# Kernel tuning notes

Hardware: AMD Instinct MI355X
Metric: run time of the kernel (lower is better)

Reference implementation:

```python
import jax, jax.numpy as jnp
import numpy as np


def setup_inputs() -> dict:
    key = jax.random.key(0)
    k1, k2, k3, k4 = jax.random.split(key, 4)
    n_smps, n_fcns, d_in, d_out = 16384, 2048, 32, 32
    GAIN = 1e-5  # xavier gain used by init_wts / init_offsets
    x = jax.random.normal(k1, (n_smps, d_in), dtype=jnp.float32)
    ctrs = jax.random.normal(k2, (n_fcns, d_in), dtype=jnp.float32)
    wts = jax.random.normal(k3, (n_fcns, d_in, d_out), dtype=jnp.float32) * GAIN
    offsets = jax.random.normal(k4, (n_fcns, d_out), dtype=jnp.float32) * GAIN
    return {"x": x, "ctrs": ctrs, "wts": wts, "offsets": offsets, "k": 4}


def reference(x, ctrs, wts, offsets, k):
    # --- knn_do equivalent (done under no_grad in torch) ---
    # squared Euclidean distance: (n_smps, n_fcns)
    x_sg = jax.lax.stop_gradient(x)
    c_sg = jax.lax.stop_gradient(ctrs)
    d2 = (jnp.sum(x_sg * x_sg, axis=1, keepdims=True)
          - 2.0 * (x_sg @ c_sg.T)
          + jnp.sum(c_sg * c_sg, axis=1)[None, :])
    _, idx = jax.lax.top_k(-d2, k)  # (n_smps, k), nearest centers

    # --- gather per-neighbor local linear models ---
    sel_wts = wts[idx]        # (n_smps, k, d_in, d_out)
    sel_ctrs = ctrs[idx]      # (n_smps, k, d_in)
    sel_offs = offsets[idx]   # (n_smps, k, d_out)

    applied_wts = jnp.sum(sel_wts, axis=1)  # (n_smps, d_in, d_out)
    # offsets minus sum over neighbors/d_in of wts * ctrs
    applied_offsets = (jnp.sum(sel_offs, axis=1)
                       - jnp.einsum('nkde,nkd->ne', sel_wts, sel_ctrs))
    # y = x @ applied_wts + applied_offsets, per sample
    y = jnp.einsum('nde,nd->ne', applied_wts, x) + applied_offsets
    return y
```

## Files before the change

kernel.cpp:

```cpp
#include <hip/hip_runtime.h>
#include <math.h>

typedef short bf16x8 __attribute__((ext_vector_type(8)));
typedef float f32x4  __attribute__((ext_vector_type(4)));

#define N_SMPS 16384
#define N_FCNS 2048
#define D_IN 32
#define D_OUT 32
#define KNN 4
#define SPLITS 4
#define CPS 512
#define TILES 32
#define POOL 48

__device__ __forceinline__ unsigned umin_u(unsigned a, unsigned b) { return a < b ? a : b; }
__device__ __forceinline__ unsigned umax_u(unsigned a, unsigned b) { return a > b ? a : b; }

__device__ __forceinline__ unsigned short bf16_rne(float f) {
  unsigned b = __float_as_uint(f);
  unsigned r = b + 0x7FFFu + ((b >> 16) & 1u);
  return (unsigned short)(r >> 16);
}

#define OFF_XH   0u
#define OFF_CH   1048576u
#define OFF_HB   (OFF_CH + 131072u)
#define OFF_WB   (OFF_HB + 8192u)
#define OFF_POOL (OFF_WB + 4194304u)

#define NX4 (N_SMPS * D_IN / 4)
#define NC4 (N_FCNS * D_IN / 4)
#define NW4 (N_FCNS * D_IN * D_OUT / 4)
#define NTOT (NX4 + NC4 + NW4)

__global__ __launch_bounds__(256) void k_prep(
    const float* __restrict__ x, const float* __restrict__ ctrs,
    const float* __restrict__ wts,
    unsigned short* __restrict__ xh, unsigned short* __restrict__ ch,
    unsigned short* __restrict__ wb, float* __restrict__ hb)
{
  const int gt = blockIdx.x * 256 + threadIdx.x;
  const float* src; unsigned short* dst; int i4;
  if (gt < NX4)            { src = x;    dst = xh; i4 = gt; }
  else if (gt < NX4 + NC4) { src = ctrs; dst = ch; i4 = gt - NX4; }
  else                     { src = wts;  dst = wb; i4 = gt - (NX4 + NC4); }
  float4 v = ((const float4*)src)[i4];
  ushort4 o;
  o.x = bf16_rne(v.x); o.y = bf16_rne(v.y);
  o.z = bf16_rne(v.z); o.w = bf16_rne(v.w);
  ((ushort4*)dst)[i4] = o;

  if (gt < N_FCNS) {
    const float4* cp4 = (const float4*)(ctrs + (size_t)gt * D_IN);
    float a = 0.f;
    #pragma unroll
    for (int q = 0; q < 8; ++q) {
      float4 c = cp4[q];
      a += c.x * c.x + c.y * c.y + c.z * c.z + c.w * c.w;
    }
    hb[gt] = -0.5f * a;
  }
}

__global__ __launch_bounds__(256) void k_topk(
    const unsigned short* __restrict__ xh, const unsigned short* __restrict__ ch,
    const float* __restrict__ hb, unsigned* __restrict__ pool)
{
  __shared__ unsigned s_cand[SPLITS][16][16][4];

  const int tid = threadIdx.x;
  const int lane = tid & 63;
  const int w = __builtin_amdgcn_readfirstlane(tid >> 6);
  const int col = lane & 15;
  const int quad = lane >> 4;
  const int sbase = blockIdx.x * 16;
  const int nbase0 = w * CPS;

  const bf16x8 ah =
      *(const bf16x8*)(xh + (size_t)(sbase + col) * D_IN + quad * 8);

  unsigned ls[4][4];
  #pragma unroll
  for (int r = 0; r < 4; ++r)
    #pragma unroll
    for (int e = 0; e < 4; ++e) ls[r][e] = 0u;

  const unsigned short* chb = ch + (size_t)nbase0 * D_IN + (size_t)col * D_IN + quad * 8;
  #define BLOAD(t) (*(const bf16x8*)(chb + (size_t)(t) * 16 * D_IN))
  #define HLOAD(t) (hb[nbase0 + (t) * 16 + col])

  bf16x8 bh0 = BLOAD(0), bh1 = BLOAD(1);
  float  hv0 = HLOAD(0), hv1 = HLOAD(1);

  for (int t = 0; t < TILES; t += 2) {
    const int tp0 = (t + 2) & (TILES - 1);
    const int tp1 = (t + 3) & (TILES - 1);
    bf16x8 bhn0 = BLOAD(tp0), bhn1 = BLOAD(tp1);
    float  hvn0 = HLOAD(tp0), hvn1 = HLOAD(tp1);

    {
      f32x4 acc = {0.f, 0.f, 0.f, 0.f};
      acc = __builtin_amdgcn_mfma_f32_16x16x32_bf16(ah, bh0, acc, 0, 0, 0);
      const unsigned tc = (unsigned)(t * 16 + col);
      #pragma unroll
      for (int r = 0; r < 4; ++r) {
        const float u = acc[r] + hv0;
        unsigned b = __float_as_uint(u);
        unsigned m = b ^ ((unsigned)((int)b >> 31) | 0x80000000u);
        unsigned key = (m & 0xFFFFFE00u) | tc;
        unsigned t0 = umin_u(ls[r][0], key); ls[r][0] = umax_u(ls[r][0], key);
        unsigned t1 = umin_u(ls[r][1], t0);  ls[r][1] = umax_u(ls[r][1], t0);
        unsigned t2 = umin_u(ls[r][2], t1);  ls[r][2] = umax_u(ls[r][2], t1);
        ls[r][3] = umax_u(ls[r][3], t2);
      }
    }
    {
      f32x4 acc = {0.f, 0.f, 0.f, 0.f};
      acc = __builtin_amdgcn_mfma_f32_16x16x32_bf16(ah, bh1, acc, 0, 0, 0);
      const unsigned tc = (unsigned)((t + 1) * 16 + col);
      #pragma unroll
      for (int r = 0; r < 4; ++r) {
        const float u = acc[r] + hv1;
        unsigned b = __float_as_uint(u);
        unsigned m = b ^ ((unsigned)((int)b >> 31) | 0x80000000u);
        unsigned key = (m & 0xFFFFFE00u) | tc;
        unsigned t0 = umin_u(ls[r][0], key); ls[r][0] = umax_u(ls[r][0], key);
        unsigned t1 = umin_u(ls[r][1], t0);  ls[r][1] = umax_u(ls[r][1], t0);
        unsigned t2 = umin_u(ls[r][2], t1);  ls[r][2] = umax_u(ls[r][2], t1);
        ls[r][3] = umax_u(ls[r][3], t2);
      }
    }
    bh0 = bhn0; bh1 = bhn1; hv0 = hvn0; hv1 = hvn1;
  }
  #undef BLOAD
  #undef HLOAD

  #pragma unroll
  for (int r = 0; r < 4; ++r) {
    const int row = quad * 4 + r;
    *(uint4*)&s_cand[w][row][col][0] =
        make_uint4(ls[r][0], ls[r][1], ls[r][2], ls[r][3]);
  }
  __syncthreads();

  if (tid < 128) {
    const int sl = tid >> 3;
    const int g  = tid & 7;
    const int wv = g >> 1;
    const int chh = (g & 1) * 8;
    unsigned q0 = 0, q1 = 0, q2 = 0, q3 = 0, q4 = 0, q5 = 0;
    #pragma unroll
    for (int c2 = 0; c2 < 8; ++c2) {
      uint4 kv = *(const uint4*)&s_cand[wv][sl][chh + c2][0];
      unsigned ks[4] = {kv.x, kv.y, kv.z, kv.w};
      #pragma unroll
      for (int e = 0; e < 4; ++e) {
        unsigned key = ks[e];
        unsigned t0 = umin_u(q0, key); q0 = umax_u(q0, key);
        unsigned t1 = umin_u(q1, t0);  q1 = umax_u(q1, t0);
        unsigned t2 = umin_u(q2, t1);  q2 = umax_u(q2, t1);
        unsigned t3 = umin_u(q3, t2);  q3 = umax_u(q3, t2);
        unsigned t4 = umin_u(q4, t3);  q4 = umax_u(q4, t3);
        q5 = umax_u(q5, t4);
      }
    }
    unsigned* op = pool + (size_t)(sbase + sl) * POOL + g * 6;
    op[0] = q0; op[1] = q1; op[2] = q2;
    op[3] = q3; op[4] = q4; op[5] = q5;
  }
}

#define K2_BLOCK 256
#define K2_SAMPLES 8

__global__ __launch_bounds__(K2_BLOCK) void k_apply(
    const float* __restrict__ x, const float* __restrict__ ctrs,
    const unsigned short* __restrict__ wb, const float* __restrict__ offs,
    const unsigned* __restrict__ pool, float* __restrict__ y)
{
  __shared__ double s_pd2[K2_SAMPLES][POOL];
  __shared__ int    s_pix[K2_SAMPLES][POOL];
  __shared__ int    s_sel[K2_SAMPLES][KNN];
  __shared__ float  s_diff[K2_SAMPLES][KNN][D_IN + 1];
  __shared__ float4 s_part[K2_SAMPLES][KNN][D_OUT / 4];

  const int tid = threadIdx.x;
  const int sbase = blockIdx.x * K2_SAMPLES;

  for (int c = tid; c < K2_SAMPLES * POOL; c += K2_BLOCK) {
    const int sl = c / POOL;
    const int p = c - sl * POOL;
    const unsigned key = pool[(size_t)(sbase + sl) * POOL + p];
    const int wv = p / 12;
    const int j = wv * CPS + (int)(key & 0x1FFu);
    const float4* xp4 = (const float4*)(x + (size_t)(sbase + sl) * D_IN);
    const float4* cp4 = (const float4*)(ctrs + (size_t)j * D_IN);
    double d2a = 0.0, d2b = 0.0;
    #pragma unroll
    for (int q = 0; q < 8; ++q) {
      float4 cv = cp4[q];
      float4 xv = xp4[q];
      double df0 = (double)xv.x - (double)cv.x;
      double df1 = (double)xv.y - (double)cv.y;
      double df2 = (double)xv.z - (double)cv.z;
      double df3 = (double)xv.w - (double)cv.w;
      d2a = fma(df0, df0, d2a);
      d2b = fma(df1, df1, d2b);
      d2a = fma(df2, df2, d2a);
      d2b = fma(df3, df3, d2b);
    }
    s_pd2[sl][p] = d2a + d2b;
    s_pix[sl][p] = j;
  }
  __syncthreads();

  if (tid < K2_SAMPLES) {
    double bd[4]; int b4[4];
    #pragma unroll
    for (int e = 0; e < 4; ++e) { bd[e] = 1e300; b4[e] = 0x7fffffff; }
    for (int m = 0; m < POOL; ++m) {
      const double d2 = s_pd2[tid][m];
      const int j = s_pix[tid][m];
      bool ins = (d2 < bd[3]) || (d2 == bd[3] && j < b4[3]);
      if (ins) {
        bd[3] = d2; b4[3] = j;
        #pragma unroll
        for (int q = 3; q > 0; --q) {
          bool sw = (bd[q] < bd[q - 1]) ||
                    (bd[q] == bd[q - 1] && b4[q] < b4[q - 1]);
          if (sw) {
            double td = bd[q]; bd[q] = bd[q - 1]; bd[q - 1] = td;
            int    tj = b4[q]; b4[q] = b4[q - 1]; b4[q - 1] = tj;
          }
        }
      }
    }
    #pragma unroll
    for (int q = 0; q < 4; ++q) s_sel[tid][q] = b4[q];
  }
  __syncthreads();

  #pragma unroll
  for (int r = 0; r < K2_SAMPLES * KNN * D_IN / K2_BLOCK; ++r) {
    int v = r * K2_BLOCK + tid;
    int d = v & 31; int p = v >> 5;
    int sl = p >> 2; int j = p & 3;
    int f = s_sel[sl][j];
    s_diff[sl][j][d] =
        x[(size_t)(sbase + sl) * D_IN + d] - ctrs[(size_t)f * D_IN + d];
  }
  __syncthreads();

  const int sl = tid >> 5;
  const int j  = (tid >> 3) & 3;
  const int eq = tid & 7;
  const int s = sbase + sl;

  const int f = s_sel[sl][j];
  const uint2* wp = (const uint2*)(wb + (size_t)f * (D_IN * D_OUT));
  float4 acc = ((const float4*)(offs + (size_t)f * D_OUT))[eq];
  #pragma unroll
  for (int d = 0; d < D_IN; ++d) {
    uint2 wv = wp[d * 8 + eq];
    float w0 = __uint_as_float(wv.x << 16);
    float w1 = __uint_as_float(wv.x & 0xFFFF0000u);
    float w2 = __uint_as_float(wv.y << 16);
    float w3 = __uint_as_float(wv.y & 0xFFFF0000u);
    float xc = s_diff[sl][j][d];
    acc.x = fmaf(xc, w0, acc.x);
    acc.y = fmaf(xc, w1, acc.y);
    acc.z = fmaf(xc, w2, acc.z);
    acc.w = fmaf(xc, w3, acc.w);
  }
  s_part[sl][j][eq] = acc;
  __syncthreads();

  if (j == 0) {
    float4 a = s_part[sl][0][eq], b = s_part[sl][1][eq];
    float4 c = s_part[sl][2][eq], e = s_part[sl][3][eq];
    float4 o;
    o.x = (a.x + b.x) + (c.x + e.x);
    o.y = (a.y + b.y) + (c.y + e.y);
    o.z = (a.z + b.z) + (c.z + e.z);
    o.w = (a.w + b.w) + (c.w + e.w);
    ((float4*)(y + (size_t)s * D_OUT))[eq] = o;
  }
}

extern "C" void kernel_launch(void* const* d_in, const int* in_sizes, int n_in,
                              void* d_out, int out_size, void* d_ws, size_t ws_size,
                              hipStream_t stream) {
  const float* x    = (const float*)d_in[0];
  const float* ctrs = (const float*)d_in[1];
  const float* wts  = (const float*)d_in[2];
  const float* offs = (const float*)d_in[3];
  float* y = (float*)d_out;

  char* ws = (char*)d_ws;
  unsigned short* xh = (unsigned short*)(ws + OFF_XH);
  unsigned short* ch = (unsigned short*)(ws + OFF_CH);
  float*          hb = (float*)(ws + OFF_HB);
  unsigned short* wb = (unsigned short*)(ws + OFF_WB);
  unsigned*     pool = (unsigned*)(ws + OFF_POOL);

  k_prep<<<NTOT / 256, 256, 0, stream>>>(x, ctrs, wts, xh, ch, wb, hb);
  k_topk<<<N_SMPS / 16, 256, 0, stream>>>(xh, ch, hb, pool);
  k_apply<<<N_SMPS / K2_SAMPLES, K2_BLOCK, 0, stream>>>(x, ctrs, wb, offs,
                                                        pool, y);
}
```

Before: 115.4 us.

## Fuse top-k candidate search and apply kernels into one mega kernel

Merges the MFMA-based candidate top-k kernel with the refine-and-apply kernel so the per-sample candidate pool stays in shared memory instead of round-tripping through global memory. Each block now handles 16 samples end to end, with a shared-memory union reused for candidates, diffs and partials. This removes one launch and the pool traffic. In exchange it raises LDS use per block, which may lower occupancy, and puts the serial refine stage in the same block as the MFMA stage.

```diff
diff --git a/kernel.cpp b/kernel.cpp
--- a/kernel.cpp
+++ b/kernel.cpp
@@ -13,6 +13,7 @@
 #define CPS 512
 #define TILES 32
 #define POOL 48
+#define SMP 16
 
 __device__ __forceinline__ unsigned umin_u(unsigned a, unsigned b) { return a < b ? a : b; }
 __device__ __forceinline__ unsigned umax_u(unsigned a, unsigned b) { return a > b ? a : b; }
@@ -27,7 +28,6 @@
 #define OFF_CH   1048576u
 #define OFF_HB   (OFF_CH + 131072u)
 #define OFF_WB   (OFF_HB + 8192u)
-#define OFF_POOL (OFF_WB + 4194304u)
 
 #define NX4 (N_SMPS * D_IN / 4)
 #define NC4 (N_FCNS * D_IN / 4)
@@ -63,18 +63,29 @@
   }
 }
 
-__global__ __launch_bounds__(256) void k_topk(
+__global__ __launch_bounds__(256) void k_mega(
     const unsigned short* __restrict__ xh, const unsigned short* __restrict__ ch,
-    const float* __restrict__ hb, unsigned* __restrict__ pool)
+    const float* __restrict__ hb,
+    const float* __restrict__ x, const float* __restrict__ ctrs,
+    const unsigned short* __restrict__ wb, const float* __restrict__ offs,
+    float* __restrict__ y)
 {
-  __shared__ unsigned s_cand[SPLITS][16][16][4];
+  __shared__ __align__(16) char u_mem[16640];
+  __shared__ unsigned s_pool[SMP][POOL];
+  __shared__ double   s_pd2[SMP][POOL];
+  __shared__ int      s_pix[SMP][POOL];
+  __shared__ int      s_sel[SMP][KNN];
+
+  unsigned* s_cand = (unsigned*)u_mem;
+  float*    s_diff = (float*)u_mem;
+  float4*   s_part = (float4*)(u_mem + 8448);
 
   const int tid = threadIdx.x;
   const int lane = tid & 63;
   const int w = __builtin_amdgcn_readfirstlane(tid >> 6);
   const int col = lane & 15;
   const int quad = lane >> 4;
-  const int sbase = blockIdx.x * 16;
+  const int sbase = blockIdx.x * SMP;
   const int nbase0 = w * CPS;
 
   const bf16x8 ah =
@@ -86,7 +97,8 @@
     #pragma unroll
     for (int e = 0; e < 4; ++e) ls[r][e] = 0u;
 
-  const unsigned short* chb = ch + (size_t)nbase0 * D_IN + (size_t)col * D_IN + quad * 8;
+  const unsigned short* chb =
+      ch + (size_t)nbase0 * D_IN + (size_t)col * D_IN + quad * 8;
   #define BLOAD(t) (*(const bf16x8*)(chb + (size_t)(t) * 16 * D_IN))
   #define HLOAD(t) (hb[nbase0 + (t) * 16 + col])
 
@@ -98,15 +110,14 @@
     const int tp1 = (t + 3) & (TILES - 1);
     bf16x8 bhn0 = BLOAD(tp0), bhn1 = BLOAD(tp1);
     float  hvn0 = HLOAD(tp0), hvn1 = HLOAD(tp1);
-
     {
       f32x4 acc = {0.f, 0.f, 0.f, 0.f};
       acc = __builtin_amdgcn_mfma_f32_16x16x32_bf16(ah, bh0, acc, 0, 0, 0);
       const unsigned tc = (unsigned)(t * 16 + col);
       #pragma unroll
       for (int r = 0; r < 4; ++r) {
-        const float u = acc[r] + hv0;
-        unsigned b = __float_as_uint(u);
+        const float uu = acc[r] + hv0;
+        unsigned b = __float_as_uint(uu);
         unsigned m = b ^ ((unsigned)((int)b >> 31) | 0x80000000u);
         unsigned key = (m & 0xFFFFFE00u) | tc;
         unsigned t0 = umin_u(ls[r][0], key); ls[r][0] = umax_u(ls[r][0], key);
@@ -121,8 +132,8 @@
       const unsigned tc = (unsigned)((t + 1) * 16 + col);
       #pragma unroll
       for (int r = 0; r < 4; ++r) {
-        const float u = acc[r] + hv1;
-        unsigned b = __float_as_uint(u);
+        const float uu = acc[r] + hv1;
+        unsigned b = __float_as_uint(uu);
         unsigned m = b ^ ((unsigned)((int)b >> 31) | 0x80000000u);
         unsigned key = (m & 0xFFFFFE00u) | tc;
         unsigned t0 = umin_u(ls[r][0], key); ls[r][0] = umax_u(ls[r][0], key);
@@ -139,7 +150,7 @@
   #pragma unroll
   for (int r = 0; r < 4; ++r) {
     const int row = quad * 4 + r;
-    *(uint4*)&s_cand[w][row][col][0] =
+    *(uint4*)&s_cand[(((w * 16) + row) * 16 + col) * 4] =
         make_uint4(ls[r][0], ls[r][1], ls[r][2], ls[r][3]);
   }
   __syncthreads();
@@ -152,7 +163,7 @@
     unsigned q0 = 0, q1 = 0, q2 = 0, q3 = 0, q4 = 0, q5 = 0;
     #pragma unroll
     for (int c2 = 0; c2 < 8; ++c2) {
-      uint4 kv = *(const uint4*)&s_cand[wv][sl][chh + c2][0];
+      uint4 kv = *(const uint4*)&s_cand[(((wv * 16) + sl) * 16 + chh + c2) * 4];
       unsigned ks[4] = {kv.x, kv.y, kv.z, kv.w};
       #pragma unroll
       for (int e = 0; e < 4; ++e) {
@@ -165,33 +176,16 @@
         q5 = umax_u(q5, t4);
       }
     }
-    unsigned* op = pool + (size_t)(sbase + sl) * POOL + g * 6;
+    unsigned* op = &s_pool[sl][g * 6];
     op[0] = q0; op[1] = q1; op[2] = q2;
     op[3] = q3; op[4] = q4; op[5] = q5;
   }
-}
-
-#define K2_BLOCK 256
-#define K2_SAMPLES 8
-
-__global__ __launch_bounds__(K2_BLOCK) void k_apply(
-    const float* __restrict__ x, const float* __restrict__ ctrs,
-    const unsigned short* __restrict__ wb, const float* __restrict__ offs,
-    const unsigned* __restrict__ pool, float* __restrict__ y)
-{
-  __shared__ double s_pd2[K2_SAMPLES][POOL];
-  __shared__ int    s_pix[K2_SAMPLES][POOL];
-  __shared__ int    s_sel[K2_SAMPLES][KNN];
-  __shared__ float  s_diff[K2_SAMPLES][KNN][D_IN + 1];
-  __shared__ float4 s_part[K2_SAMPLES][KNN][D_OUT / 4];
-
-  const int tid = threadIdx.x;
-  const int sbase = blockIdx.x * K2_SAMPLES;
-
-  for (int c = tid; c < K2_SAMPLES * POOL; c += K2_BLOCK) {
+  __syncthreads();
+
+  for (int c = tid; c < SMP * POOL; c += 256) {
     const int sl = c / POOL;
     const int p = c - sl * POOL;
-    const unsigned key = pool[(size_t)(sbase + sl) * POOL + p];
+    const unsigned key = s_pool[sl][p];
     const int wv = p / 12;
     const int j = wv * CPS + (int)(key & 0x1FFu);
     const float4* xp4 = (const float4*)(x + (size_t)(sbase + sl) * D_IN);
@@ -215,7 +209,7 @@
   }
   __syncthreads();
 
-  if (tid < K2_SAMPLES) {
+  if (tid < SMP) {
     double bd[4]; int b4[4];
     #pragma unroll
     for (int e = 0; e < 4; ++e) { bd[e] = 1e300; b4[e] = 0x7fffffff; }
@@ -242,49 +236,60 @@
   __syncthreads();
 
   #pragma unroll
-  for (int r = 0; r < K2_SAMPLES * KNN * D_IN / K2_BLOCK; ++r) {
-    int v = r * K2_BLOCK + tid;
+  for (int r = 0; r < SMP * KNN * D_IN / 256; ++r) {
+    int v = r * 256 + tid;
     int d = v & 31; int p = v >> 5;
     int sl = p >> 2; int j = p & 3;
     int f = s_sel[sl][j];
-    s_diff[sl][j][d] =
+    s_diff[(sl * KNN + j) * (D_IN + 1) + d] =
         x[(size_t)(sbase + sl) * D_IN + d] - ctrs[(size_t)f * D_IN + d];
   }
   __syncthreads();
 
-  const int sl = tid >> 5;
-  const int j  = (tid >> 3) & 3;
-  const int eq = tid & 7;
-  const int s = sbase + sl;
-
-  const int f = s_sel[sl][j];
-  const uint2* wp = (const uint2*)(wb + (size_t)f * (D_IN * D_OUT));
-  float4 acc = ((const float4*)(offs + (size_t)f * D_OUT))[eq];
-  #pragma unroll
-  for (int d = 0; d < D_IN; ++d) {
-    uint2 wv = wp[d * 8 + eq];
-    float w0 = __uint_as_float(wv.x << 16);
-    float w1 = __uint_as_float(wv.x & 0xFFFF0000u);
-    float w2 = __uint_as_float(wv.y << 16);
-    float w3 = __uint_as_float(wv.y & 0xFFFF0000u);
-    float xc = s_diff[sl][j][d];
-    acc.x = fmaf(xc, w0, acc.x);
-    acc.y = fmaf(xc, w1, acc.y);
-    acc.z = fmaf(xc, w2, acc.z);
-    acc.w = fmaf(xc, w3, acc.w);
-  }
-  s_part[sl][j][eq] = acc;
-  __syncthreads();
-
-  if (j == 0) {
-    float4 a = s_part[sl][0][eq], b = s_part[sl][1][eq];
-    float4 c = s_part[sl][2][eq], e = s_part[sl][3][eq];
-    float4 o;
-    o.x = (a.x + b.x) + (c.x + e.x);
-    o.y = (a.y + b.y) + (c.y + e.y);
-    o.z = (a.z + b.z) + (c.z + e.z);
-    o.w = (a.w + b.w) + (c.w + e.w);
-    ((float4*)(y + (size_t)s * D_OUT))[eq] = o;
+  #pragma unroll
+  for (int r = 0; r < 2; ++r) {
+    const int slot = r * 256 + tid;
+    const int sl = slot >> 5;
+    const int j  = (slot >> 3) & 3;
+    const int eq = slot & 7;
+    const int f = s_sel[sl][j];
+    const uint2* wp = (const uint2*)(wb + (size_t)f * (D_IN * D_OUT));
+    float4 acc = ((const float4*)(offs + (size_t)f * D_OUT))[eq];
+    #pragma unroll
+    for (int d = 0; d < D_IN; ++d) {
+      uint2 wv = wp[d * 8 + eq];
+      float w0 = __uint_as_float(wv.x << 16);
+      float w1 = __uint_as_float(wv.x & 0xFFFF0000u);
+      float w2 = __uint_as_float(wv.y << 16);
+      float w3 = __uint_as_float(wv.y & 0xFFFF0000u);
+      float xc = s_diff[(sl * KNN + j) * (D_IN + 1) + d];
+      acc.x = fmaf(xc, w0, acc.x);
+      acc.y = fmaf(xc, w1, acc.y);
+      acc.z = fmaf(xc, w2, acc.z);
+      acc.w = fmaf(xc, w3, acc.w);
+    }
+    s_part[(sl * KNN + j) * 8 + eq] = acc;
+  }
+  __syncthreads();
+
+  #pragma unroll
+  for (int r = 0; r < 2; ++r) {
+    const int slot = r * 256 + tid;
+    const int sl = slot >> 5;
+    const int j  = (slot >> 3) & 3;
+    const int eq = slot & 7;
+    if (j == 0) {
+      float4 a = s_part[(sl * KNN + 0) * 8 + eq];
+      float4 b = s_part[(sl * KNN + 1) * 8 + eq];
+      float4 c = s_part[(sl * KNN + 2) * 8 + eq];
+      float4 e = s_part[(sl * KNN + 3) * 8 + eq];
+      float4 o;
+      o.x = (a.x + b.x) + (c.x + e.x);
+      o.y = (a.y + b.y) + (c.y + e.y);
+      o.z = (a.z + b.z) + (c.z + e.z);
+      o.w = (a.w + b.w) + (c.w + e.w);
+      ((float4*)(y + (size_t)(sbase + sl) * D_OUT))[eq] = o;
+    }
   }
 }
 
@@ -302,10 +307,7 @@
   unsigned short* ch = (unsigned short*)(ws + OFF_CH);
   float*          hb = (float*)(ws + OFF_HB);
   unsigned short* wb = (unsigned short*)(ws + OFF_WB);
-  unsigned*     pool = (unsigned*)(ws + OFF_POOL);
 
   k_prep<<<NTOT / 256, 256, 0, stream>>>(x, ctrs, wts, xh, ch, wb, hb);
-  k_topk<<<N_SMPS / 16, 256, 0, stream>>>(xh, ch, hb, pool);
-  k_apply<<<N_SMPS / K2_SAMPLES, K2_BLOCK, 0, stream>>>(x, ctrs, wb, offs,
-                                                        pool, y);
+  k_mega<<<N_SMPS / SMP, 256, 0, stream>>>(xh, ch, hb, x, ctrs, wb, offs, y);
 }
```

New measurement: 114.5 us. About the same (-0.7%).
